# Kernel optimization log

Measured on AMD Instinct MI355X. Metric: run time of the kernel, lower is better.

The kernel has to match this reference:

```python
import jax, jax.numpy as jnp
import numpy as np

LAYERS = 2      # LightGCN propagation layers
LAMB = 0.5      # aux loss weight
REG = 1e-4      # embedding reg weight
N_AUX = 2       # len(behaviors) - 1


def setup_inputs() -> dict:
    key = jax.random.key(0)
    k = jax.random.split(key, 8)
    n_users, n_items, d = 100000, 50000, 32
    E = 1000000
    user_emb = (jax.random.normal(k[0], (n_users + 1, d), jnp.float32) * 0.1).at[0].set(0.0)
    item_emb = (jax.random.normal(k[1], (n_items + 1, d), jnp.float32) * 0.1).at[0].set(0.0)
    aux_u = jax.random.randint(k[2], (N_AUX, E), 1, n_users + 1)
    aux_i = jax.random.randint(k[3], (N_AUX, E), 1, n_items + 1)
    aux_edges = jnp.stack([aux_u, aux_i], axis=-1).astype(jnp.int32)
    tgt_u = jax.random.randint(k[4], (E,), 1, n_users + 1)
    tgt_i = jax.random.randint(k[5], (E,), 1, n_items + 1)
    target_edges = jnp.stack([tgt_u, tgt_i], axis=-1).astype(jnp.int32)
    # [B, 1+N_AUX, 3]: per row (user, pos_item, neg_item) for target then each aux behavior
    batch_data = jax.random.randint(k[6], (4096, 1 + N_AUX, 3), 1, n_items + 1).astype(jnp.int32)
    return {"user_emb": user_emb, "item_emb": item_emb, "batch_data": batch_data,
            "aux_edges": aux_edges, "target_edges": target_edges}


def _graph(edges, n_user_rows, N):
    """Symmetric-normalized bipartite LightGCN graph as directed COO (src, dst, w)."""
    u = edges[:, 0]
    v = edges[:, 1] + n_user_rows  # shift item ids into joint node space
    ones = jnp.ones(u.shape[0], jnp.float32)
    deg = jax.ops.segment_sum(ones, u, num_segments=N) + jax.ops.segment_sum(ones, v, num_segments=N)
    dinv = jnp.where(deg > 0, jax.lax.rsqrt(jnp.maximum(deg, 1.0)), 0.0)
    w = dinv[u] * dinv[v]
    src = jnp.concatenate([u, v])
    dst = jnp.concatenate([v, u])
    w2 = jnp.concatenate([w, w])
    return src, dst, w2


def _lightgcn(emb, src, dst, w, N):
    """L-layer LightGCN propagation, mean over layers 0..L."""
    acc = emb
    cur = emb
    for _ in range(LAYERS):
        cur = jax.ops.segment_sum(w[:, None] * cur[src], dst, num_segments=N)
        acc = acc + cur
    return acc / (LAYERS + 1)


def _prob(ue, ie, u, i):
    return jax.nn.relu(jnp.sum(ue[u] * ie[i], axis=-1))


def _bpr(p, n):
    return -jnp.mean(jax.nn.log_sigmoid(p - n))


def reference(user_emb, item_emb, batch_data, aux_edges, target_edges):
    Nu = user_emb.shape[0]
    N = Nu + item_emb.shape[0]
    all_emb = jnp.concatenate([user_emb, item_emb], axis=0)
    tgt_g = _graph(target_edges, Nu, N)

    user, p_item, n_item = batch_data[:, 0, 0], batch_data[:, 0, 1], batch_data[:, 0, 2]
    aux_user, aux_p, aux_n = batch_data[:, 1:, 0], batch_data[:, 1:, 1], batch_data[:, 1:, 2]

    cps, cns, dps, dns, aps, ans, aux_losses = [], [], [], [], [], [], []
    for idx in range(N_AUX):
        # combine graph = aux behavior edges union target edges
        comb_edges = jnp.concatenate([aux_edges[idx], target_edges], axis=0)
        ce = _lightgcn(all_emb, *_graph(comb_edges, Nu, N), N)
        cu, ci = ce[:Nu], ce[Nu:]
        cps.append(_prob(cu, ci, user, p_item))
        cns.append(_prob(cu, ci, user, n_item))

        ae = _lightgcn(all_emb, *_graph(aux_edges[idx], Nu, N), N)
        au, ai = ae[:Nu], ae[Nu:]
        aps.append(_prob(au, ai, user, p_item))
        ans.append(_prob(au, ai, user, n_item))

        # condition: propagate aux embeddings through the target graph
        de = _lightgcn(ae, *tgt_g, N)
        du, di = de[:Nu], de[Nu:]
        dps.append(_prob(du, di, user, p_item))
        dns.append(_prob(du, di, user, n_item))

        ps = jnp.sum(au[aux_user[:, idx]] * ai[aux_p[:, idx]], axis=-1)
        ns = jnp.sum(au[aux_user[:, idx]] * ai[aux_n[:, idx]], axis=-1)
        aux_losses.append(_bpr(ps, ns))

    aux_loss = jnp.mean(jnp.stack(aux_losses))

    def front_door(cond, comb, aux):
        return jnp.sum(cond * jnp.sum(comb * aux, axis=0), axis=0)

    p_scores = front_door(jnp.stack(dps), jnp.stack(cps), jnp.stack(aps))
    n_scores = front_door(jnp.stack(dns), jnp.stack(cns), jnp.stack(ans))
    rec_loss = _bpr(p_scores, n_scores)
    emb_loss = (jnp.linalg.norm(user_emb) + jnp.linalg.norm(item_emb)) / item_emb.shape[0]
    return rec_loss + LAMB * aux_loss + REG * emb_loss
```

## Files before the change

### kernel.cpp

```cpp
#include <hip/hip_runtime.h>
#include <hip/hip_fp16.h>
#include <math.h>

#define D 32
#define ROWU 16
#define NBK 1024
#define BSHIFT 8
#define TILE_H 16384
#define TILE_BIN 2048

typedef unsigned int u32;
typedef unsigned short u16;

__device__ __forceinline__ float logsigf(float x) {
  return fminf(x, 0.f) - log1pf(expf(-fabsf(x)));
}

__device__ __forceinline__ float lo16(u32 u) { return __uint_as_float(u << 16); }
__device__ __forceinline__ float hi16(u32 u) { return __uint_as_float(u & 0xFFFF0000u); }
__device__ __forceinline__ u32 pk2(float a, float b) {
  u32 ua = __float_as_uint(a), ub = __float_as_uint(b);
  u32 ra = (ua + 0x7FFFu + ((ua >> 16) & 1u)) >> 16;
  u32 rb = (ub + 0x7FFFu + ((ub >> 16) & 1u)) >> 16;
  return (ra & 0xFFFFu) | (rb << 16);
}
__device__ __forceinline__ float bfat(const u16* __restrict__ p, size_t off) {
  return __uint_as_float(((u32)p[off]) << 16);
}
__device__ __forceinline__ void accum8(float* a, float w, uint4 x) {
  a[0] += w * lo16(x.x); a[1] += w * hi16(x.x);
  a[2] += w * lo16(x.y); a[3] += w * hi16(x.y);
  a[4] += w * lo16(x.z); a[5] += w * hi16(x.z);
  a[6] += w * lo16(x.w); a[7] += w * hi16(x.w);
}
__device__ __forceinline__ uint4 pack8(const float* a, float w) {
  return make_uint4(pk2(w * a[0], w * a[1]), pk2(w * a[2], w * a[3]),
                    pk2(w * a[4], w * a[5]), pk2(w * a[6], w * a[7]));
}

__device__ __forceinline__ u32 wpack(float a, float b) {
  __half2 h = __floats2half2_rn(a, b);
  return *reinterpret_cast<u32*>(&h);
}
__device__ __forceinline__ float2 hun(int wb) {
  __half2 h;
  *reinterpret_cast<int*>(&h) = wb;
  return __half22float2(h);
}


__global__ void hist_kernel(const int2* __restrict__ tgt, const int2* __restrict__ aux,
                            int E, int Nu, int BPS, int* __restrict__ bcur) {
  __shared__ int lh[NBK];
  int seg = blockIdx.x / BPS;
  int blk = blockIdx.x - seg * BPS;
  const int2* edges = (seg == 0) ? tgt : aux + (size_t)(seg - 1) * E;
  for (int b = threadIdx.x; b < NBK; b += 256) lh[b] = 0;
  __syncthreads();
  int e0 = blk * TILE_H;
  for (int k = threadIdx.x; k < TILE_H; k += 256) {
    int e = e0 + k;
    if (e < E) {
      int2 ed = edges[e];
      atomicAdd(&lh[ed.x >> BSHIFT], 1);
      atomicAdd(&lh[(ed.y + Nu) >> BSHIFT], 1);
    }
  }
  __syncthreads();
  for (int b = threadIdx.x; b < NBK; b += 256)
    if (lh[b]) atomicAdd(&bcur[seg * NBK + b], lh[b]);
}

__global__ void bscan_kernel(int* __restrict__ bcur) {
  int* b = bcur + blockIdx.x * NBK;
  int lane = threadIdx.x;
  int carry = 0;
  for (int base = 0; base < NBK; base += 64) {
    int i = base + lane;
    int v = b[i];
    int s = v;
    #pragma unroll
    for (int o = 1; o < 64; o <<= 1) {
      int t = __shfl_up(s, o);
      if (lane >= o) s += t;
    }
    b[i] = carry + s - v;
    carry += __shfl(s, 63);
  }
}

__global__ void bin_kernel(const int2* __restrict__ tgt, const int2* __restrict__ aux,
                           int E, int Nu, int BPS, int* __restrict__ bcur,
                           int* __restrict__ binned) {
  __shared__ int lh[NBK];
  __shared__ int gb[NBK];
  int seg = blockIdx.x / BPS;
  int blk = blockIdx.x - seg * BPS;
  const int2* edges = (seg == 0) ? tgt : aux + (size_t)(seg - 1) * E;
  int* out = binned + (size_t)seg * 2 * E;
  int tid = threadIdx.x;
  for (int b = tid; b < NBK; b += 256) lh[b] = 0;
  __syncthreads();
  int e0 = blk * TILE_BIN;
  int pkv[16];
  int pb[16];
  int pr[16];
  #pragma unroll
  for (int it = 0; it < 8; ++it) {
    int e = e0 + tid + it * 256;
    bool ok = e < E;
    int2 ed = ok ? edges[e] : make_int2(0, -Nu);
    int u = ed.x, v = ed.y + Nu;
    int b1 = u >> BSHIFT, b2 = v >> BSHIFT;
    pkv[2 * it] = ((u & 255) << 18) | v;
    pb[2 * it] = b1;
    pr[2 * it] = ok ? atomicAdd(&lh[b1], 1) : 0;
    pkv[2 * it + 1] = ((v & 255) << 18) | u;
    pb[2 * it + 1] = b2;
    pr[2 * it + 1] = ok ? atomicAdd(&lh[b2], 1) : 0;
  }
  __syncthreads();
  #pragma unroll
  for (int j = 0; j < 4; ++j) {
    int b = tid * 4 + j;
    int c = lh[b];
    gb[b] = c ? atomicAdd(&bcur[seg * NBK + b], c) : 0;
  }
  __syncthreads();
  #pragma unroll
  for (int it = 0; it < 16; ++it) {
    int e = e0 + tid + (it >> 1) * 256;
    if (e < E) out[gb[pb[it]] + pr[it]] = pkv[it];
  }
}

__global__ void csr_count_kernel(const int* __restrict__ binned,
                                 const int* __restrict__ bend, int E2, int N, int NBKe,
                                 int* __restrict__ deg3, int* __restrict__ rp3) {
  __shared__ int cnt[256];
  __shared__ int wred[4];
  int seg = blockIdx.x / NBKe;
  int bkt = blockIdx.x - seg * NBKe;
  int node0 = bkt << BSHIFT;
  const int* bc = bend + seg * NBK;
  int start = (bkt == 0) ? 0 : bc[bkt - 1];
  int end = bc[bkt];
  int cntE = end - start;
  const int* src = binned + (size_t)seg * E2 + start;
  cnt[threadIdx.x] = 0;
  __syncthreads();
  for (int k = threadIdx.x; k < cntE; k += 256) atomicAdd(&cnt[src[k] >> 18], 1);
  __syncthreads();
  int lane = threadIdx.x & 63, wid = threadIdx.x >> 6;
  int v = cnt[threadIdx.x];
  int incl = v;
  #pragma unroll
  for (int o = 1; o < 64; o <<= 1) {
    int t = __shfl_up(incl, o);
    if (lane >= o) incl += t;
  }
  if (lane == 63) wred[wid] = incl;
  __syncthreads();
  int wbase = 0;
  for (int w = 0; w < wid; ++w) wbase += wred[w];
  int node = node0 + (int)threadIdx.x;
  if (node < N) {
    deg3[(size_t)seg * N + node] = v;
    rp3[(size_t)seg * (N + 1) + node] = start + wbase + incl - v;
  }
  if (bkt == 0 && threadIdx.x == 0) rp3[(size_t)seg * (N + 1) + N] = E2;
}

__global__ void dinv_all_kernel(const int* __restrict__ deg3, float* __restrict__ dinv5,
                                u32* __restrict__ wtab, int N) {
  int n = blockIdx.x * blockDim.x + threadIdx.x;
  if (n >= N) return;
  int dt = deg3[n], d0 = deg3[N + n], d1 = deg3[2 * N + n];
  float wt  = dt ? rsqrtf((float)dt) : 0.f;
  float wa0 = d0 ? rsqrtf((float)d0) : 0.f;
  float wa1 = d1 ? rsqrtf((float)d1) : 0.f;
  int c0 = dt + d0, c1 = dt + d1;
  float wc0 = c0 ? rsqrtf((float)c0) : 0.f;
  float wc1 = c1 ? rsqrtf((float)c1) : 0.f;
  dinv5[n] = wt;
  dinv5[N + n] = wa0;
  dinv5[2 * N + n] = wa1;
  dinv5[3 * N + n] = wc0;
  dinv5[4 * N + n] = wc1;
  wtab[n] = wpack(wc0, wc1);
  wtab[N + n] = wpack(wa0, wc0);
  wtab[2 * N + n] = wpack(wa1, wc1);
}

__global__ void csr_scatter_kernel(const int* __restrict__ binned,
                                   const int* __restrict__ bend,
                                   const int* __restrict__ rp3,
                                   const u32* __restrict__ wtab,
                                   int E2, int N, int NBKe,
                                   int2* __restrict__ pk) {
  __shared__ int cnt[256];
  __shared__ int off[256];
  int seg = blockIdx.x / NBKe;
  int bkt = blockIdx.x - seg * NBKe;
  int node0 = bkt << BSHIFT;
  const int* bc = bend + seg * NBK;
  int start = (bkt == 0) ? 0 : bc[bkt - 1];
  int end = bc[bkt];
  int cntE = end - start;
  const int* src = binned + (size_t)seg * E2 + start;
  int node = node0 + (int)threadIdx.x;
  off[threadIdx.x] = (node < N) ? rp3[(size_t)seg * (N + 1) + node] : 0;
  cnt[threadIdx.x] = 0;
  const u32* wt = wtab + (size_t)seg * N;
  __syncthreads();
  int2* out = pk + (size_t)seg * E2;
  for (int k = threadIdx.x; k < cntE; k += 256) {
    int en = src[k];
    int lb = en >> 18;
    int c = en & 0x3FFFF;
    int pos = atomicAdd(&cnt[lb], 1);
    out[off[lb] + pos] = make_int2(c, (int)wt[c]);
  }
}

__global__ void cvt_emb_kernel(const float2* __restrict__ ue, long nu2,
                               const float2* __restrict__ ie, long ni2,
                               u32* __restrict__ emb) {
  long i = (long)blockIdx.x * blockDim.x + threadIdx.x;
  if (i >= nu2 + ni2) return;
  float2 v = (i < nu2) ? ue[i] : ie[i - nu2];
  emb[i] = pk2(v.x, v.y);
}


__device__ __forceinline__ void edge1_dual(const int2* __restrict__ p, int j, int lane,
                                           const uint4* __restrict__ rows,
                                           float* a1, float* a2) {
  int2 en = p[j];
  float2 w = hun(en.y);
  uint4 x = rows[(size_t)en.x * 4 + lane];
  accum8(a1, w.x, x);
  accum8(a2, w.y, x);
}

__device__ __forceinline__ void stream_dual(const int* __restrict__ rp,
                                            const int2* __restrict__ p, int n, int lane,
                                            const uint4* __restrict__ rows,
                                            float* a1, float* a2) {
  int j = rp[n], e = rp[n + 1];
  if ((j & 1) && j < e) { edge1_dual(p, j, lane, rows, a1, a2); ++j; }
  for (; j + 3 < e; j += 4) {
    int4 m0 = *reinterpret_cast<const int4*>(p + j);
    int4 m1 = *reinterpret_cast<const int4*>(p + j + 2);
    uint4 x0 = rows[(size_t)m0.x * 4 + lane];
    uint4 x1 = rows[(size_t)m0.z * 4 + lane];
    uint4 x2 = rows[(size_t)m1.x * 4 + lane];
    uint4 x3 = rows[(size_t)m1.z * 4 + lane];
    float2 w0 = hun(m0.y), w1 = hun(m0.w), w2 = hun(m1.y), w3 = hun(m1.w);
    accum8(a1, w0.x, x0); accum8(a2, w0.y, x0);
    accum8(a1, w1.x, x1); accum8(a2, w1.y, x1);
    accum8(a1, w2.x, x2); accum8(a2, w2.y, x2);
    accum8(a1, w3.x, x3); accum8(a2, w3.y, x3);
  }
  for (; j < e; ++j) edge1_dual(p, j, lane, rows, a1, a2);
}

__global__ void gather_fused_all_kernel(const int* __restrict__ rp3,
                                        const int2* __restrict__ pk,
                                        const float* __restrict__ dinv5,
                                        const uint4* __restrict__ emb,
                                        uint4* __restrict__ BaAll, uint4* __restrict__ BcAll,
                                        int N, int E2) {
  const int* rpA0 = rp3 + (size_t)(N + 1);
  const int* rpA1 = rp3 + 2 * (size_t)(N + 1);
  const int2* pT = pk;
  const int2* pA0 = pk + (size_t)E2;
  const int2* pA1 = pk + 2 * (size_t)E2;
  const float* dvA0 = dinv5 + (size_t)N;
  const float* dvA1 = dinv5 + 2 * (size_t)N;
  const float* dvC0 = dinv5 + 3 * (size_t)N;
  const float* dvC1 = dinv5 + 4 * (size_t)N;
  int t = blockIdx.x * blockDim.x + threadIdx.x;
  int n = t >> 2;
  if (n >= N) return;
  int lane = t & 3;
  float aA0[8] = {0, 0, 0, 0, 0, 0, 0, 0};
  float aA1[8] = {0, 0, 0, 0, 0, 0, 0, 0};
  float aC0[8] = {0, 0, 0, 0, 0, 0, 0, 0};
  float aC1[8] = {0, 0, 0, 0, 0, 0, 0, 0};
  stream_dual(rpA0, pA0, n, lane, emb, aA0, aC0);
  stream_dual(rpA1, pA1, n, lane, emb, aA1, aC1);
  stream_dual(rp3, pT, n, lane, emb, aC0, aC1);
  size_t o = (size_t)n * 4 + lane;
  size_t rowN4 = (size_t)N * 4;
  BaAll[o] = pack8(aA0, dvA0[n]);
  BaAll[rowN4 + o] = pack8(aA1, dvA1[n]);
  BcAll[o] = pack8(aC0, dvC0[n]);
  BcAll[rowN4 + o] = pack8(aC1, dvC1[n]);
}

__global__ void gather_avg_kernel(const int* __restrict__ rp3, const int2* __restrict__ pk,
                                  const float* __restrict__ dinv5,
                                  const uint4* __restrict__ emb,
                                  const uint4* __restrict__ BaAll, uint4* __restrict__ AI,
                                  int N, int E2) {
  int idx = blockIdx.y;
  const int* rp = rp3 + (size_t)(1 + idx) * (N + 1);
  const int2* pA = pk + (size_t)(1 + idx) * E2;
  const float* dv = dinv5 + (size_t)(1 + idx) * N;
  const uint4* cur = BaAll + (size_t)idx * N * 4;
  int t = blockIdx.x * blockDim.x + threadIdx.x;
  int n = t >> 2;
  if (n >= N) return;
  int lane = t & 3;
  float acc[8] = {0, 0, 0, 0, 0, 0, 0, 0};
  int j = rp[n], e = rp[n + 1];
  if ((j & 1) && j < e) {
    int2 en = pA[j];
    uint4 x = cur[(size_t)en.x * 4 + lane];
    accum8(acc, hun(en.y).x, x);
    ++j;
  }
  for (; j + 3 < e; j += 4) {
    int4 m0 = *reinterpret_cast<const int4*>(pA + j);
    int4 m1 = *reinterpret_cast<const int4*>(pA + j + 2);
    uint4 x0 = cur[(size_t)m0.x * 4 + lane];
    uint4 x1 = cur[(size_t)m0.z * 4 + lane];
    uint4 x2 = cur[(size_t)m1.x * 4 + lane];
    uint4 x3 = cur[(size_t)m1.z * 4 + lane];
    accum8(acc, hun(m0.y).x, x0);
    accum8(acc, hun(m0.w).x, x1);
    accum8(acc, hun(m1.y).x, x2);
    accum8(acc, hun(m1.w).x, x3);
  }
  for (; j < e; ++j) {
    int2 en = pA[j];
    uint4 x = cur[(size_t)en.x * 4 + lane];
    accum8(acc, hun(en.y).x, x);
  }
  float wn = dv[n];
  uint4 e4 = emb[(size_t)n * 4 + lane];
  uint4 b4 = cur[(size_t)n * 4 + lane];
  float r[8];
  r[0] = (lo16(e4.x) + lo16(b4.x) + wn * acc[0]) * (1.f / 3.f);
  r[1] = (hi16(e4.x) + hi16(b4.x) + wn * acc[1]) * (1.f / 3.f);
  r[2] = (lo16(e4.y) + lo16(b4.y) + wn * acc[2]) * (1.f / 3.f);
  r[3] = (hi16(e4.y) + hi16(b4.y) + wn * acc[3]) * (1.f / 3.f);
  r[4] = (lo16(e4.z) + lo16(b4.z) + wn * acc[4]) * (1.f / 3.f);
  r[5] = (hi16(e4.z) + hi16(b4.z) + wn * acc[5]) * (1.f / 3.f);
  r[6] = (lo16(e4.w) + lo16(b4.w) + wn * acc[6]) * (1.f / 3.f);
  r[7] = (hi16(e4.w) + hi16(b4.w) + wn * acc[7]) * (1.f / 3.f);
  AI[(size_t)n * 8 + idx * 4 + lane] = pack8(r, 1.f);
}

__global__ void de_gather_kernel(const int* __restrict__ rp3, const int2* __restrict__ pk,
                                 const float* __restrict__ dinv5,
                                 const uint4* __restrict__ AI, uint4* __restrict__ DeI,
                                 int N) {
  int t = blockIdx.x * blockDim.x + threadIdx.x;
  int n = t >> 3;
  if (n >= N) return;
  int lane = t & 7;
  float acc[8] = {0, 0, 0, 0, 0, 0, 0, 0};
  int j = rp3[n], e = rp3[n + 1];
  if ((j & 1) && j < e) {
    int c = pk[j].x;
    uint4 x = AI[(size_t)c * 8 + lane];
    accum8(acc, dinv5[c], x);
    ++j;
  }
  for (; j + 3 < e; j += 4) {
    int4 m0 = *reinterpret_cast<const int4*>(pk + j);
    int4 m1 = *reinterpret_cast<const int4*>(pk + j + 2);
    uint4 x0 = AI[(size_t)m0.x * 8 + lane];
    uint4 x1 = AI[(size_t)m0.z * 8 + lane];
    uint4 x2 = AI[(size_t)m1.x * 8 + lane];
    uint4 x3 = AI[(size_t)m1.z * 8 + lane];
    accum8(acc, dinv5[m0.x], x0);
    accum8(acc, dinv5[m0.z], x1);
    accum8(acc, dinv5[m1.x], x2);
    accum8(acc, dinv5[m1.z], x3);
  }
  for (; j < e; ++j) {
    int c = pk[j].x;
    uint4 x = AI[(size_t)c * 8 + lane];
    accum8(acc, dinv5[c], x);
  }
  DeI[(size_t)n * 8 + lane] = pack8(acc, dinv5[n]);
}


__device__ __forceinline__ float fdim2(const int2* __restrict__ pkA, const int2* __restrict__ pkT,
                                       const int* __restrict__ rpA, const int* __restrict__ rpT,
                                       int idx, const float* __restrict__ dv,
                                       const u16* __restrict__ base, const u16* __restrict__ L1,
                                       int r, int d) {
  float acc = 0.f;
  for (int j = rpA[r]; j < rpA[r + 1]; ++j) {
    int2 en = pkA[j];
    acc += hun(en.y).y * bfat(L1, (size_t)en.x * D + d);
  }
  for (int j = rpT[r]; j < rpT[r + 1]; ++j) {
    int2 en = pkT[j];
    float2 w = hun(en.y);
    acc += (idx ? w.y : w.x) * bfat(L1, (size_t)en.x * D + d);
  }
  return (bfat(base, (size_t)r * D + d) + bfat(L1, (size_t)r * D + d) + dv[r] * acc) * (1.f / 3.f);
}

__device__ __forceinline__ float fdim1i(const int2* __restrict__ pkT, const int* __restrict__ rp,
                                        const float* __restrict__ dv,
                                        const u16* __restrict__ base, const u16* __restrict__ L1,
                                        int r, int di) {
  float acc = 0.f;
  for (int j = rp[r]; j < rp[r + 1]; ++j) {
    int2 en = pkT[j];
    acc += dv[en.x] * bfat(L1, (size_t)en.x * 64 + di);
  }
  return (bfat(base, (size_t)r * 64 + di) + bfat(L1, (size_t)r * 64 + di) + dv[r] * acc) * (1.f / 3.f);
}

__global__ void ce_sparse_kernel(const int* __restrict__ rp3, const int2* __restrict__ pk,
                                 const float* __restrict__ dinv5,
                                 const u32* __restrict__ EMBu, const u32* __restrict__ BcAll,
                                 const int* __restrict__ batch, int Bsz, int Nu, int N, int E2,
                                 float* __restrict__ cps, float* __restrict__ cns) {
  int idx = blockIdx.y;
  const int* rpA = rp3 + (size_t)(1 + idx) * (N + 1);
  const int2* pkA = pk + (size_t)(1 + idx) * E2;
  const float* dv = dinv5 + (size_t)(3 + idx) * N;
  const u16* base = (const u16*)EMBu;
  const u16* L1 = (const u16*)(BcAll + (size_t)idx * N * ROWU);
  float* outp = cps + (size_t)idx * Bsz;
  float* outn = cns + (size_t)idx * Bsz;
  int t = blockIdx.x * blockDim.x + threadIdx.x;
  int b = t >> 5, d = t & 31;
  if (b >= Bsz) return;
  int u = batch[b * 9 + 0];
  int p = batch[b * 9 + 1] + Nu;
  int n = batch[b * 9 + 2] + Nu;
  float uv = fdim2(pkA, pk, rpA, rp3, idx, dv, base, L1, u, d);
  float pv = fdim2(pkA, pk, rpA, rp3, idx, dv, base, L1, p, d);
  float nv = fdim2(pkA, pk, rpA, rp3, idx, dv, base, L1, n, d);
  float sp = uv * pv, sn = uv * nv;
  #pragma unroll
  for (int o = 16; o > 0; o >>= 1) {
    sp += __shfl_down(sp, o, 32);
    sn += __shfl_down(sn, o, 32);
  }
  if (d == 0) {
    outp[b] = fmaxf(sp, 0.f);
    outn[b] = fmaxf(sn, 0.f);
  }
}

__global__ void de_sparse_kernel(const int* __restrict__ rp3, const int2* __restrict__ pk,
                                 const float* __restrict__ dinv5,
                                 const u32* __restrict__ AI, const u32* __restrict__ DeI,
                                 const int* __restrict__ batch, int Bsz, int Nu, int N,
                                 float* __restrict__ dps, float* __restrict__ dns) {
  int idx = blockIdx.y;
  const u16* base = (const u16*)AI;
  const u16* L1 = (const u16*)DeI;
  float* outp = dps + (size_t)idx * Bsz;
  float* outn = dns + (size_t)idx * Bsz;
  int t = blockIdx.x * blockDim.x + threadIdx.x;
  int b = t >> 5, d = t & 31;
  if (b >= Bsz) return;
  int di = idx * 32 + d;
  int u = batch[b * 9 + 0];
  int p = batch[b * 9 + 1] + Nu;
  int n = batch[b * 9 + 2] + Nu;
  float uv = fdim1i(pk, rp3, dinv5, base, L1, u, di);
  float pv = fdim1i(pk, rp3, dinv5, base, L1, p, di);
  float nv = fdim1i(pk, rp3, dinv5, base, L1, n, di);
  float sp = uv * pv, sn = uv * nv;
  #pragma unroll
  for (int o = 16; o > 0; o >>= 1) {
    sp += __shfl_down(sp, o, 32);
    sn += __shfl_down(sn, o, 32);
  }
  if (d == 0) {
    outp[b] = fmaxf(sp, 0.f);
    outn[b] = fmaxf(sn, 0.f);
  }
}


__device__ __forceinline__ float dotrow(const u32* __restrict__ a, const u32* __restrict__ b) {
  float s = 0.f;
  #pragma unroll
  for (int k = 0; k < ROWU; ++k) {
    u32 x = a[k], y = b[k];
    s += lo16(x) * lo16(y) + hi16(x) * hi16(y);
  }
  return s;
}

__global__ void score_aux_kernel(const u32* __restrict__ AI, const int* __restrict__ batch,
                                 int Bsz, int Nu, int N, float* __restrict__ aps,
                                 float* __restrict__ ans_, float* __restrict__ accs) {
  int idx = blockIdx.y;
  const u32* A = AI + (size_t)idx * ROWU;
  float* outp = aps + (size_t)idx * Bsz;
  float* outn = ans_ + (size_t)idx * Bsz;
  int b = blockIdx.x * blockDim.x + threadIdx.x;
  float l = 0.f;
  if (b < Bsz) {
    int u = batch[b * 9 + 0];
    int p = batch[b * 9 + 1] + Nu;
    int n = batch[b * 9 + 2] + Nu;
    const u32* ur = A + (size_t)u * 32;
    outp[b] = fmaxf(dotrow(ur, A + (size_t)p * 32), 0.f);
    outn[b] = fmaxf(dotrow(ur, A + (size_t)n * 32), 0.f);
    const int* r = batch + b * 9 + 3 * (1 + idx);
    const u32* aur = A + (size_t)r[0] * 32;
    float ps = dotrow(aur, A + (size_t)(r[1] + Nu) * 32);
    float ns = dotrow(aur, A + (size_t)(r[2] + Nu) * 32);
    l = -logsigf(ps - ns);
  }
  for (int o = 32; o > 0; o >>= 1) l += __shfl_down(l, o);
  if ((threadIdx.x & 63) == 0) atomicAdd(&accs[idx], l);
}

__global__ void recloss_kernel(const float* __restrict__ cps, const float* __restrict__ cns,
                               const float* __restrict__ aps, const float* __restrict__ ans_,
                               const float* __restrict__ dps, const float* __restrict__ dns,
                               int Bsz, int NA, float* __restrict__ acc) {
  int b = blockIdx.x * blockDim.x + threadIdx.x;
  float l = 0.f;
  if (b < Bsz) {
    float dp = 0.f, dn = 0.f, cap = 0.f, can = 0.f;
    for (int i = 0; i < NA; ++i) {
      dp += dps[i * Bsz + b];
      dn += dns[i * Bsz + b];
      cap += cps[i * Bsz + b] * aps[i * Bsz + b];
      can += cns[i * Bsz + b] * ans_[i * Bsz + b];
    }
    l = -logsigf(dp * cap - dn * can);
  }
  for (int o = 32; o > 0; o >>= 1) l += __shfl_down(l, o);
  if ((threadIdx.x & 63) == 0) atomicAdd(acc, l);
}

__global__ void sumsq2_kernel(const float4* __restrict__ xu, int n4u,
                              const float4* __restrict__ xi, int n4i,
                              float* __restrict__ accU, float* __restrict__ accI) {
  __shared__ float redU[4], redI[4];
  int tid = threadIdx.x;
  int gid = blockIdx.x * blockDim.x + tid;
  int stride = gridDim.x * blockDim.x;
  float su = 0.f, si = 0.f;
  for (int i = gid; i < n4u; i += stride) {
    float4 v = xu[i];
    su += v.x * v.x + v.y * v.y + v.z * v.z + v.w * v.w;
  }
  for (int i = gid; i < n4i; i += stride) {
    float4 v = xi[i];
    si += v.x * v.x + v.y * v.y + v.z * v.z + v.w * v.w;
  }
  for (int o = 32; o > 0; o >>= 1) {
    su += __shfl_down(su, o);
    si += __shfl_down(si, o);
  }
  if ((tid & 63) == 0) { redU[tid >> 6] = su; redI[tid >> 6] = si; }
  __syncthreads();
  if (tid == 0) {
    atomicAdd(accU, redU[0] + redU[1] + redU[2] + redU[3]);
    atomicAdd(accI, redI[0] + redI[1] + redI[2] + redI[3]);
  }
}

__global__ void final_kernel(const float* __restrict__ accs, int Bsz, int NA, int NiRows,
                             float* __restrict__ out) {
  float rec = accs[NA] / (float)Bsz;
  float aux = 0.f;
  for (int i = 0; i < NA; ++i) aux += accs[i] / (float)Bsz;
  aux /= (float)NA;
  float embl = (sqrtf(accs[NA + 1]) + sqrtf(accs[NA + 2])) / (float)NiRows;
  out[0] = rec + 0.5f * aux + 1e-4f * embl;
}

extern "C" void kernel_launch(void* const* d_in, const int* in_sizes, int n_in,
                              void* d_out, int out_size, void* d_ws, size_t ws_size,
                              hipStream_t stream) {
  const float* user_emb = (const float*)d_in[0];
  const float* item_emb = (const float*)d_in[1];
  const int* batch = (const int*)d_in[2];
  const int* aux_edges = (const int*)d_in[3];
  const int* tgt_edges = (const int*)d_in[4];

  const int NuRows = in_sizes[0] / D;
  const int NiRows = in_sizes[1] / D;
  const int Bsz = in_sizes[2] / 9;
  const int E = in_sizes[4] / 2;
  const int NA = in_sizes[3] / (2 * E);
  const int N = NuRows + NiRows;
  const int E2 = 2 * E;
  const size_t rowH = (size_t)N * ROWU;
  const int BPS_H = (E + TILE_H - 1) / TILE_H;
  const int BPS_B = (E + TILE_BIN - 1) / TILE_BIN;
  const int NBKe = (N + (1 << BSHIFT) - 1) >> BSHIFT;

  u32* EMBu = (u32*)d_ws;
  u32* AI = EMBu + rowH;
  u32* BaAll = AI + 2 * rowH;
  u32* BcAll = BaAll + 2 * rowH;
  int* deg3 = (int*)(BcAll + 2 * rowH);
  float* dinv5 = (float*)(deg3 + 3 * (size_t)N);
  u32* wtab = (u32*)(dinv5 + 5 * (size_t)N);
  int* rp3 = (int*)(wtab + 3 * (size_t)N);
  int* bcur = rp3 + 3 * (size_t)(N + 1);
  uintptr_t pka = ((uintptr_t)(bcur + 3 * (size_t)NBK) + 15) & ~(uintptr_t)15;
  int2* pk = (int2*)pka;
  float* cps = (float*)(pk + 3 * (size_t)E2);
  float* cns = cps + (size_t)NA * Bsz;
  float* aps = cns + (size_t)NA * Bsz;
  float* ans_ = aps + (size_t)NA * Bsz;
  float* dps = ans_ + (size_t)NA * Bsz;
  float* dns = dps + (size_t)NA * Bsz;
  float* accs = dns + (size_t)NA * Bsz;
  int* binned = (int*)AI;

  const int TB = 256;
  const int gN = (N + TB - 1) / TB;
  const int gN4 = (N * 4 + TB - 1) / TB;
  const int gN8 = (N * 8 + TB - 1) / TB;
  const int gB = (Bsz + TB - 1) / TB;
  const int gB32 = (Bsz * 32 + TB - 1) / TB;
  const long nu2 = (long)NuRows * ROWU;
  const long ni2 = (long)NiRows * ROWU;
  const int gCvt = (int)((nu2 + ni2 + TB - 1) / TB);

  cvt_emb_kernel<<<gCvt, TB, 0, stream>>>((const float2*)user_emb, nu2,
                                          (const float2*)item_emb, ni2, EMBu);

  hipMemsetAsync(bcur, 0, 3 * (size_t)NBK * sizeof(int), stream);
  hist_kernel<<<3 * BPS_H, TB, 0, stream>>>((const int2*)tgt_edges, (const int2*)aux_edges,
                                            E, NuRows, BPS_H, bcur);
  bscan_kernel<<<3, 64, 0, stream>>>(bcur);
  bin_kernel<<<3 * BPS_B, TB, 0, stream>>>((const int2*)tgt_edges, (const int2*)aux_edges,
                                           E, NuRows, BPS_B, bcur, binned);
  csr_count_kernel<<<3 * NBKe, TB, 0, stream>>>(binned, bcur, E2, N, NBKe, deg3, rp3);
  dinv_all_kernel<<<gN, TB, 0, stream>>>(deg3, dinv5, wtab, N);
  csr_scatter_kernel<<<3 * NBKe, TB, 0, stream>>>(binned, bcur, rp3, wtab, E2, N, NBKe, pk);

  hipMemsetAsync(accs, 0, (size_t)(NA + 3) * sizeof(float), stream);

  dim3 gridG(gN4, NA), gridB(gB, NA), gridS(gB32, NA);

  gather_fused_all_kernel<<<gN4, TB, 0, stream>>>(rp3, pk, dinv5, (const uint4*)EMBu,
                                                  (uint4*)BaAll, (uint4*)BcAll, N, E2);
  gather_avg_kernel<<<gridG, TB, 0, stream>>>(rp3, pk, dinv5, (const uint4*)EMBu,
                                              (const uint4*)BaAll, (uint4*)AI, N, E2);
  score_aux_kernel<<<gridB, TB, 0, stream>>>(AI, batch, Bsz, NuRows, N, aps, ans_, accs);
  ce_sparse_kernel<<<gridS, TB, 0, stream>>>(rp3, pk, dinv5, EMBu, BcAll,
                                             batch, Bsz, NuRows, N, E2, cps, cns);
  de_gather_kernel<<<gN8, TB, 0, stream>>>(rp3, pk, dinv5, (const uint4*)AI,
                                           (uint4*)BaAll, N);
  de_sparse_kernel<<<gridS, TB, 0, stream>>>(rp3, pk, dinv5, AI, (const u32*)BaAll,
                                             batch, Bsz, NuRows, N, dps, dns);

  sumsq2_kernel<<<104, TB, 0, stream>>>((const float4*)user_emb,
                                        (int)((size_t)NuRows * D / 4),
                                        (const float4*)item_emb,
                                        (int)((size_t)NiRows * D / 4),
                                        accs + NA + 1, accs + NA + 2);
  recloss_kernel<<<gB, TB, 0, stream>>>(cps, cns, aps, ans_, dps, dns, Bsz, NA, accs + NA);
  final_kernel<<<1, 1, 0, stream>>>(accs, Bsz, NA, NiRows, (float*)d_out);
}
```

Baseline: 626.8 us.

## Merge independent small kernels into shared launches to cut launch count

Packs several independent kernels into single launches that dispatch on block index. The embedding bf16 conversion rides along with the histogram kernel and now converts float4 at a time. The aux gather/average is interleaved with the ce_sparse scoring. The aux score, sum-of-squares and de-gather share one launch, and recloss plus final become one single-block kernel. This removes about five launches and their serialization gaps, at the cost of heterogeneous blocks in one grid and a single-block final reduction.

```diff
diff --git a/kernel.cpp b/kernel.cpp
--- a/kernel.cpp
+++ b/kernel.cpp
@@ -8,6 +8,7 @@
 #define BSHIFT 8
 #define TILE_H 16384
 #define TILE_BIN 2048
+#define SQB 104
 
 typedef unsigned int u32;
 typedef unsigned short u16;
@@ -49,11 +50,24 @@
 }
 
 
-__global__ void hist_kernel(const int2* __restrict__ tgt, const int2* __restrict__ aux,
-                            int E, int Nu, int BPS, int* __restrict__ bcur) {
+__global__ void hist_cvt_kernel(const int2* __restrict__ tgt, const int2* __restrict__ aux,
+                                int E, int Nu, int BPS, int histB, int* __restrict__ bcur,
+                                const float4* __restrict__ ue, long nu2h,
+                                const float4* __restrict__ ie, long ni2h,
+                                u32* __restrict__ emb) {
   __shared__ int lh[NBK];
-  int seg = blockIdx.x / BPS;
-  int blk = blockIdx.x - seg * BPS;
+  int x = blockIdx.x;
+  if (x >= histB) {
+    long i2 = (long)(x - histB) * blockDim.x + threadIdx.x;
+    if (i2 < nu2h + ni2h) {
+      float4 v = (i2 < nu2h) ? ue[i2] : ie[i2 - nu2h];
+      uint2 o = make_uint2(pk2(v.x, v.y), pk2(v.z, v.w));
+      *reinterpret_cast<uint2*>(emb + 2 * i2) = o;
+    }
+    return;
+  }
+  int seg = x / BPS;
+  int blk = x - seg * BPS;
   const int2* edges = (seg == 0) ? tgt : aux + (size_t)(seg - 1) * E;
   for (int b = threadIdx.x; b < NBK; b += 256) lh[b] = 0;
   __syncthreads();
@@ -221,15 +235,6 @@
     int pos = atomicAdd(&cnt[lb], 1);
     out[off[lb] + pos] = make_int2(c, (int)wt[c]);
   }
-}
-
-__global__ void cvt_emb_kernel(const float2* __restrict__ ue, long nu2,
-                               const float2* __restrict__ ie, long ni2,
-                               u32* __restrict__ emb) {
-  long i = (long)blockIdx.x * blockDim.x + threadIdx.x;
-  if (i >= nu2 + ni2) return;
-  float2 v = (i < nu2) ? ue[i] : ie[i - nu2];
-  emb[i] = pk2(v.x, v.y);
 }
 
 
@@ -299,17 +304,18 @@
   BcAll[rowN4 + o] = pack8(aC1, dvC1[n]);
 }
 
-__global__ void gather_avg_kernel(const int* __restrict__ rp3, const int2* __restrict__ pk,
+
+__device__ __forceinline__ void gather_avg_body(int bx, int idx,
+                                  const int* __restrict__ rp3, const int2* __restrict__ pk,
                                   const float* __restrict__ dinv5,
                                   const uint4* __restrict__ emb,
                                   const uint4* __restrict__ BaAll, uint4* __restrict__ AI,
                                   int N, int E2) {
-  int idx = blockIdx.y;
   const int* rp = rp3 + (size_t)(1 + idx) * (N + 1);
   const int2* pA = pk + (size_t)(1 + idx) * E2;
   const float* dv = dinv5 + (size_t)(1 + idx) * N;
   const uint4* cur = BaAll + (size_t)idx * N * 4;
-  int t = blockIdx.x * blockDim.x + threadIdx.x;
+  int t = bx * 256 + threadIdx.x;
   int n = t >> 2;
   if (n >= N) return;
   int lane = t & 3;
@@ -353,43 +359,6 @@
   AI[(size_t)n * 8 + idx * 4 + lane] = pack8(r, 1.f);
 }
 
-__global__ void de_gather_kernel(const int* __restrict__ rp3, const int2* __restrict__ pk,
-                                 const float* __restrict__ dinv5,
-                                 const uint4* __restrict__ AI, uint4* __restrict__ DeI,
-                                 int N) {
-  int t = blockIdx.x * blockDim.x + threadIdx.x;
-  int n = t >> 3;
-  if (n >= N) return;
-  int lane = t & 7;
-  float acc[8] = {0, 0, 0, 0, 0, 0, 0, 0};
-  int j = rp3[n], e = rp3[n + 1];
-  if ((j & 1) && j < e) {
-    int c = pk[j].x;
-    uint4 x = AI[(size_t)c * 8 + lane];
-    accum8(acc, dinv5[c], x);
-    ++j;
-  }
-  for (; j + 3 < e; j += 4) {
-    int4 m0 = *reinterpret_cast<const int4*>(pk + j);
-    int4 m1 = *reinterpret_cast<const int4*>(pk + j + 2);
-    uint4 x0 = AI[(size_t)m0.x * 8 + lane];
-    uint4 x1 = AI[(size_t)m0.z * 8 + lane];
-    uint4 x2 = AI[(size_t)m1.x * 8 + lane];
-    uint4 x3 = AI[(size_t)m1.z * 8 + lane];
-    accum8(acc, dinv5[m0.x], x0);
-    accum8(acc, dinv5[m0.z], x1);
-    accum8(acc, dinv5[m1.x], x2);
-    accum8(acc, dinv5[m1.z], x3);
-  }
-  for (; j < e; ++j) {
-    int c = pk[j].x;
-    uint4 x = AI[(size_t)c * 8 + lane];
-    accum8(acc, dinv5[c], x);
-  }
-  DeI[(size_t)n * 8 + lane] = pack8(acc, dinv5[n]);
-}
-
-
 __device__ __forceinline__ float fdim2(const int2* __restrict__ pkA, const int2* __restrict__ pkT,
                                        const int* __restrict__ rpA, const int* __restrict__ rpT,
                                        int idx, const float* __restrict__ dv,
@@ -408,24 +377,12 @@
   return (bfat(base, (size_t)r * D + d) + bfat(L1, (size_t)r * D + d) + dv[r] * acc) * (1.f / 3.f);
 }
 
-__device__ __forceinline__ float fdim1i(const int2* __restrict__ pkT, const int* __restrict__ rp,
-                                        const float* __restrict__ dv,
-                                        const u16* __restrict__ base, const u16* __restrict__ L1,
-                                        int r, int di) {
-  float acc = 0.f;
-  for (int j = rp[r]; j < rp[r + 1]; ++j) {
-    int2 en = pkT[j];
-    acc += dv[en.x] * bfat(L1, (size_t)en.x * 64 + di);
-  }
-  return (bfat(base, (size_t)r * 64 + di) + bfat(L1, (size_t)r * 64 + di) + dv[r] * acc) * (1.f / 3.f);
-}
-
-__global__ void ce_sparse_kernel(const int* __restrict__ rp3, const int2* __restrict__ pk,
+__device__ __forceinline__ void ce_body(int bx, int idx,
+                                 const int* __restrict__ rp3, const int2* __restrict__ pk,
                                  const float* __restrict__ dinv5,
                                  const u32* __restrict__ EMBu, const u32* __restrict__ BcAll,
                                  const int* __restrict__ batch, int Bsz, int Nu, int N, int E2,
                                  float* __restrict__ cps, float* __restrict__ cns) {
-  int idx = blockIdx.y;
   const int* rpA = rp3 + (size_t)(1 + idx) * (N + 1);
   const int2* pkA = pk + (size_t)(1 + idx) * E2;
   const float* dv = dinv5 + (size_t)(3 + idx) * N;
@@ -433,7 +390,7 @@
   const u16* L1 = (const u16*)(BcAll + (size_t)idx * N * ROWU);
   float* outp = cps + (size_t)idx * Bsz;
   float* outn = cns + (size_t)idx * Bsz;
-  int t = blockIdx.x * blockDim.x + threadIdx.x;
+  int t = bx * 256 + threadIdx.x;
   int b = t >> 5, d = t & 31;
   if (b >= Bsz) return;
   int u = batch[b * 9 + 0];
@@ -452,6 +409,145 @@
     outp[b] = fmaxf(sp, 0.f);
     outn[b] = fmaxf(sn, 0.f);
   }
+}
+
+__global__ void gather_avg_ce_kernel(const int* __restrict__ rp3, const int2* __restrict__ pk,
+                                     const float* __restrict__ dinv5,
+                                     const uint4* __restrict__ emb,
+                                     const uint4* __restrict__ BaAll, uint4* __restrict__ AI,
+                                     const u32* __restrict__ EMBu, const u32* __restrict__ BcAll,
+                                     const int* __restrict__ batch, int Bsz, int Nu,
+                                     int N, int E2, int CEB,
+                                     float* __restrict__ cps, float* __restrict__ cns) {
+  int x = blockIdx.x;
+  int idx = blockIdx.y;
+  int lim = 5 * CEB;
+  if (x < lim && (x % 5) == 4) {
+    ce_body(x / 5, idx, rp3, pk, dinv5, EMBu, BcAll, batch, Bsz, Nu, N, E2, cps, cns);
+  } else {
+    int ceBefore = (x < lim) ? ((x + 1) / 5) : CEB;
+    gather_avg_body(x - ceBefore, idx, rp3, pk, dinv5, emb, BaAll, AI, N, E2);
+  }
+}
+
+
+__device__ __forceinline__ float dotrow(const u32* __restrict__ a, const u32* __restrict__ b) {
+  float s = 0.f;
+  #pragma unroll
+  for (int k = 0; k < ROWU; ++k) {
+    u32 x = a[k], y = b[k];
+    s += lo16(x) * lo16(y) + hi16(x) * hi16(y);
+  }
+  return s;
+}
+
+__global__ void de_score_sumsq_kernel(const int* __restrict__ rp3, const int2* __restrict__ pk,
+                                      const float* __restrict__ dinv5,
+                                      const uint4* __restrict__ AI4, uint4* __restrict__ DeI,
+                                      const u32* __restrict__ AI, const int* __restrict__ batch,
+                                      int Bsz, int Nu, int N, int NA, int gBs,
+                                      float* __restrict__ aps, float* __restrict__ ans_,
+                                      float* __restrict__ accs,
+                                      const float4* __restrict__ xu, int n4u,
+                                      const float4* __restrict__ xi, int n4i) {
+  __shared__ float redU[4], redI[4];
+  int x = blockIdx.x;
+  int scoreB = gBs * NA;
+  int tid = threadIdx.x;
+  if (x < scoreB) {
+    int idx = x / gBs;
+    int bx = x - idx * gBs;
+    const u32* A = AI + (size_t)idx * ROWU;
+    float* outp = aps + (size_t)idx * Bsz;
+    float* outn = ans_ + (size_t)idx * Bsz;
+    int b = bx * 256 + tid;
+    float l = 0.f;
+    if (b < Bsz) {
+      int u = batch[b * 9 + 0];
+      int p = batch[b * 9 + 1] + Nu;
+      int n = batch[b * 9 + 2] + Nu;
+      const u32* ur = A + (size_t)u * 32;
+      outp[b] = fmaxf(dotrow(ur, A + (size_t)p * 32), 0.f);
+      outn[b] = fmaxf(dotrow(ur, A + (size_t)n * 32), 0.f);
+      const int* r = batch + b * 9 + 3 * (1 + idx);
+      const u32* aur = A + (size_t)r[0] * 32;
+      float ps = dotrow(aur, A + (size_t)(r[1] + Nu) * 32);
+      float ns = dotrow(aur, A + (size_t)(r[2] + Nu) * 32);
+      l = -logsigf(ps - ns);
+    }
+    for (int o = 32; o > 0; o >>= 1) l += __shfl_down(l, o);
+    if ((tid & 63) == 0) atomicAdd(&accs[idx], l);
+    return;
+  }
+  if (x < scoreB + SQB) {
+    int bx = x - scoreB;
+    int gid = bx * 256 + tid;
+    int stride = SQB * 256;
+    float su = 0.f, si = 0.f;
+    for (int i = gid; i < n4u; i += stride) {
+      float4 v = xu[i];
+      su += v.x * v.x + v.y * v.y + v.z * v.z + v.w * v.w;
+    }
+    for (int i = gid; i < n4i; i += stride) {
+      float4 v = xi[i];
+      si += v.x * v.x + v.y * v.y + v.z * v.z + v.w * v.w;
+    }
+    for (int o = 32; o > 0; o >>= 1) {
+      su += __shfl_down(su, o);
+      si += __shfl_down(si, o);
+    }
+    if ((tid & 63) == 0) { redU[tid >> 6] = su; redI[tid >> 6] = si; }
+    __syncthreads();
+    if (tid == 0) {
+      atomicAdd(&accs[NA + 1], redU[0] + redU[1] + redU[2] + redU[3]);
+      atomicAdd(&accs[NA + 2], redI[0] + redI[1] + redI[2] + redI[3]);
+    }
+    return;
+  }
+  int bx = x - scoreB - SQB;
+  int t = bx * 256 + tid;
+  int n = t >> 3;
+  if (n >= N) return;
+  int lane = t & 7;
+  float acc[8] = {0, 0, 0, 0, 0, 0, 0, 0};
+  int j = rp3[n], e = rp3[n + 1];
+  if ((j & 1) && j < e) {
+    int c = pk[j].x;
+    uint4 xr = AI4[(size_t)c * 8 + lane];
+    accum8(acc, dinv5[c], xr);
+    ++j;
+  }
+  for (; j + 3 < e; j += 4) {
+    int4 m0 = *reinterpret_cast<const int4*>(pk + j);
+    int4 m1 = *reinterpret_cast<const int4*>(pk + j + 2);
+    uint4 x0 = AI4[(size_t)m0.x * 8 + lane];
+    uint4 x1 = AI4[(size_t)m0.z * 8 + lane];
+    uint4 x2 = AI4[(size_t)m1.x * 8 + lane];
+    uint4 x3 = AI4[(size_t)m1.z * 8 + lane];
+    accum8(acc, dinv5[m0.x], x0);
+    accum8(acc, dinv5[m0.z], x1);
+    accum8(acc, dinv5[m1.x], x2);
+    accum8(acc, dinv5[m1.z], x3);
+  }
+  for (; j < e; ++j) {
+    int c = pk[j].x;
+    uint4 xr = AI4[(size_t)c * 8 + lane];
+    accum8(acc, dinv5[c], xr);
+  }
+  DeI[(size_t)n * 8 + lane] = pack8(acc, dinv5[n]);
+}
+
+
+__device__ __forceinline__ float fdim1i(const int2* __restrict__ pkT, const int* __restrict__ rp,
+                                        const float* __restrict__ dv,
+                                        const u16* __restrict__ base, const u16* __restrict__ L1,
+                                        int r, int di) {
+  float acc = 0.f;
+  for (int j = rp[r]; j < rp[r + 1]; ++j) {
+    int2 en = pkT[j];
+    acc += dv[en.x] * bfat(L1, (size_t)en.x * 64 + di);
+  }
+  return (bfat(base, (size_t)r * 64 + di) + bfat(L1, (size_t)r * 64 + di) + dv[r] * acc) * (1.f / 3.f);
 }
 
 __global__ void de_sparse_kernel(const int* __restrict__ rp3, const int2* __restrict__ pk,
@@ -487,49 +583,15 @@
 }
 
 
-__device__ __forceinline__ float dotrow(const u32* __restrict__ a, const u32* __restrict__ b) {
-  float s = 0.f;
-  #pragma unroll
-  for (int k = 0; k < ROWU; ++k) {
-    u32 x = a[k], y = b[k];
-    s += lo16(x) * lo16(y) + hi16(x) * hi16(y);
-  }
-  return s;
-}
-
-__global__ void score_aux_kernel(const u32* __restrict__ AI, const int* __restrict__ batch,
-                                 int Bsz, int Nu, int N, float* __restrict__ aps,
-                                 float* __restrict__ ans_, float* __restrict__ accs) {
-  int idx = blockIdx.y;
-  const u32* A = AI + (size_t)idx * ROWU;
-  float* outp = aps + (size_t)idx * Bsz;
-  float* outn = ans_ + (size_t)idx * Bsz;
-  int b = blockIdx.x * blockDim.x + threadIdx.x;
+__global__ void recloss_final_kernel(const float* __restrict__ cps, const float* __restrict__ cns,
+                                     const float* __restrict__ aps, const float* __restrict__ ans_,
+                                     const float* __restrict__ dps, const float* __restrict__ dns,
+                                     int Bsz, int NA, const float* __restrict__ accs,
+                                     int NiRows, float* __restrict__ out) {
+  __shared__ float red[4];
+  int tid = threadIdx.x;
   float l = 0.f;
-  if (b < Bsz) {
-    int u = batch[b * 9 + 0];
-    int p = batch[b * 9 + 1] + Nu;
-    int n = batch[b * 9 + 2] + Nu;
-    const u32* ur = A + (size_t)u * 32;
-    outp[b] = fmaxf(dotrow(ur, A + (size_t)p * 32), 0.f);
-    outn[b] = fmaxf(dotrow(ur, A + (size_t)n * 32), 0.f);
-    const int* r = batch + b * 9 + 3 * (1 + idx);
-    const u32* aur = A + (size_t)r[0] * 32;
-    float ps = dotrow(aur, A + (size_t)(r[1] + Nu) * 32);
-    float ns = dotrow(aur, A + (size_t)(r[2] + Nu) * 32);
-    l = -logsigf(ps - ns);
-  }
-  for (int o = 32; o > 0; o >>= 1) l += __shfl_down(l, o);
-  if ((threadIdx.x & 63) == 0) atomicAdd(&accs[idx], l);
-}
-
-__global__ void recloss_kernel(const float* __restrict__ cps, const float* __restrict__ cns,
-                               const float* __restrict__ aps, const float* __restrict__ ans_,
-                               const float* __restrict__ dps, const float* __restrict__ dns,
-                               int Bsz, int NA, float* __restrict__ acc) {
-  int b = blockIdx.x * blockDim.x + threadIdx.x;
-  float l = 0.f;
-  if (b < Bsz) {
+  for (int b = tid; b < Bsz; b += 256) {
     float dp = 0.f, dn = 0.f, cap = 0.f, can = 0.f;
     for (int i = 0; i < NA; ++i) {
       dp += dps[i * Bsz + b];
@@ -537,48 +599,19 @@
       cap += cps[i * Bsz + b] * aps[i * Bsz + b];
       can += cns[i * Bsz + b] * ans_[i * Bsz + b];
     }
-    l = -logsigf(dp * cap - dn * can);
+    l += -logsigf(dp * cap - dn * can);
   }
   for (int o = 32; o > 0; o >>= 1) l += __shfl_down(l, o);
-  if ((threadIdx.x & 63) == 0) atomicAdd(acc, l);
-}
-
-__global__ void sumsq2_kernel(const float4* __restrict__ xu, int n4u,
-                              const float4* __restrict__ xi, int n4i,
-                              float* __restrict__ accU, float* __restrict__ accI) {
-  __shared__ float redU[4], redI[4];
-  int tid = threadIdx.x;
-  int gid = blockIdx.x * blockDim.x + tid;
-  int stride = gridDim.x * blockDim.x;
-  float su = 0.f, si = 0.f;
-  for (int i = gid; i < n4u; i += stride) {
-    float4 v = xu[i];
-    su += v.x * v.x + v.y * v.y + v.z * v.z + v.w * v.w;
-  }
-  for (int i = gid; i < n4i; i += stride) {
-    float4 v = xi[i];
-    si += v.x * v.x + v.y * v.y + v.z * v.z + v.w * v.w;
-  }
-  for (int o = 32; o > 0; o >>= 1) {
-    su += __shfl_down(su, o);
-    si += __shfl_down(si, o);
-  }
-  if ((tid & 63) == 0) { redU[tid >> 6] = su; redI[tid >> 6] = si; }
+  if ((tid & 63) == 0) red[tid >> 6] = l;
   __syncthreads();
   if (tid == 0) {
-    atomicAdd(accU, redU[0] + redU[1] + redU[2] + redU[3]);
-    atomicAdd(accI, redI[0] + redI[1] + redI[2] + redI[3]);
-  }
-}
-
-__global__ void final_kernel(const float* __restrict__ accs, int Bsz, int NA, int NiRows,
-                             float* __restrict__ out) {
-  float rec = accs[NA] / (float)Bsz;
-  float aux = 0.f;
-  for (int i = 0; i < NA; ++i) aux += accs[i] / (float)Bsz;
-  aux /= (float)NA;
-  float embl = (sqrtf(accs[NA + 1]) + sqrtf(accs[NA + 2])) / (float)NiRows;
-  out[0] = rec + 0.5f * aux + 1e-4f * embl;
+    float rec = (red[0] + red[1] + red[2] + red[3]) / (float)Bsz;
+    float aux = 0.f;
+    for (int i = 0; i < NA; ++i) aux += accs[i] / (float)Bsz;
+    aux /= (float)NA;
+    float embl = (sqrtf(accs[NA + 1]) + sqrtf(accs[NA + 2])) / (float)NiRows;
+    out[0] = rec + 0.5f * aux + 1e-4f * embl;
+  }
 }
 
 extern "C" void kernel_launch(void* const* d_in, const int* in_sizes, int n_in,
@@ -630,14 +663,14 @@
   const int gB32 = (Bsz * 32 + TB - 1) / TB;
   const long nu2 = (long)NuRows * ROWU;
   const long ni2 = (long)NiRows * ROWU;
-  const int gCvt = (int)((nu2 + ni2 + TB - 1) / TB);
-
-  cvt_emb_kernel<<<gCvt, TB, 0, stream>>>((const float2*)user_emb, nu2,
-                                          (const float2*)item_emb, ni2, EMBu);
+  const long nu2h = nu2 / 2, ni2h = ni2 / 2;
+  const int gCvt2 = (int)((nu2h + ni2h + TB - 1) / TB);
+  const int histB = 3 * BPS_H;
 
   hipMemsetAsync(bcur, 0, 3 * (size_t)NBK * sizeof(int), stream);
-  hist_kernel<<<3 * BPS_H, TB, 0, stream>>>((const int2*)tgt_edges, (const int2*)aux_edges,
-                                            E, NuRows, BPS_H, bcur);
+  hist_cvt_kernel<<<histB + gCvt2, TB, 0, stream>>>(
+      (const int2*)tgt_edges, (const int2*)aux_edges, E, NuRows, BPS_H, histB, bcur,
+      (const float4*)user_emb, nu2h, (const float4*)item_emb, ni2h, EMBu);
   bscan_kernel<<<3, 64, 0, stream>>>(bcur);
   bin_kernel<<<3 * BPS_B, TB, 0, stream>>>((const int2*)tgt_edges, (const int2*)aux_edges,
                                            E, NuRows, BPS_B, bcur, binned);
@@ -647,25 +680,25 @@
 
   hipMemsetAsync(accs, 0, (size_t)(NA + 3) * sizeof(float), stream);
 
-  dim3 gridG(gN4, NA), gridB(gB, NA), gridS(gB32, NA);
-
   gather_fused_all_kernel<<<gN4, TB, 0, stream>>>(rp3, pk, dinv5, (const uint4*)EMBu,
                                                   (uint4*)BaAll, (uint4*)BcAll, N, E2);
-  gather_avg_kernel<<<gridG, TB, 0, stream>>>(rp3, pk, dinv5, (const uint4*)EMBu,
-                                              (const uint4*)BaAll, (uint4*)AI, N, E2);
-  score_aux_kernel<<<gridB, TB, 0, stream>>>(AI, batch, Bsz, NuRows, N, aps, ans_, accs);
-  ce_sparse_kernel<<<gridS, TB, 0, stream>>>(rp3, pk, dinv5, EMBu, BcAll,
-                                             batch, Bsz, NuRows, N, E2, cps, cns);
-  de_gather_kernel<<<gN8, TB, 0, stream>>>(rp3, pk, dinv5, (const uint4*)AI,
-                                           (uint4*)BaAll, N);
+
+  dim3 gridAC(gN4 + gB32, NA);
+  gather_avg_ce_kernel<<<gridAC, TB, 0, stream>>>(rp3, pk, dinv5, (const uint4*)EMBu,
+                                                  (const uint4*)BaAll, (uint4*)AI,
+                                                  EMBu, BcAll, batch, Bsz, NuRows,
+                                                  N, E2, gB32, cps, cns);
+
+  de_score_sumsq_kernel<<<gB * NA + SQB + gN8, TB, 0, stream>>>(
+      rp3, pk, dinv5, (const uint4*)AI, (uint4*)BaAll, AI, batch,
+      Bsz, NuRows, N, NA, gB, aps, ans_, accs,
+      (const float4*)user_emb, (int)((size_t)NuRows * D / 4),
+      (const float4*)item_emb, (int)((size_t)NiRows * D / 4));
+
+  dim3 gridS(gB32, NA);
   de_sparse_kernel<<<gridS, TB, 0, stream>>>(rp3, pk, dinv5, AI, (const u32*)BaAll,
                                              batch, Bsz, NuRows, N, dps, dns);
 
-  sumsq2_kernel<<<104, TB, 0, stream>>>((const float4*)user_emb,
-                                        (int)((size_t)NuRows * D / 4),
-                                        (const float4*)item_emb,
-                                        (int)((size_t)NiRows * D / 4),
-                                        accs + NA + 1, accs + NA + 2);
-  recloss_kernel<<<gB, TB, 0, stream>>>(cps, cns, aps, ans_, dps, dns, Bsz, NA, accs + NA);
-  final_kernel<<<1, 1, 0, stream>>>(accs, Bsz, NA, NiRows, (float*)d_out);
-}
+  recloss_final_kernel<<<1, TB, 0, stream>>>(cps, cns, aps, ans_, dps, dns,
+                                             Bsz, NA, accs, NiRows, (float*)d_out);
+}
```

Measured after the change: 592.6 us. -5.5%, faster.
